# Kernel tuning notes

Measured on AMD Instinct MI355X. Metric: run time of the kernel, lower is better.

## Reference

```python
import math
import jax, jax.numpy as jnp
import numpy as np

HEADS = 16
MODEL = 1024
KEY = 64
VAL = 64
B, S = 4, 2048


def setup_inputs() -> dict:
    key = jax.random.key(0)
    ks = jax.random.split(key, 8)
    queries = jax.random.normal(ks[0], (B, S, MODEL), dtype=jnp.float32)
    keys_ = jax.random.normal(ks[1], (B, S, MODEL), dtype=jnp.float32)
    values = jax.random.normal(ks[2], (B, S, MODEL), dtype=jnp.float32)
    # causal boolean mask, true = attention allowed (every row has >=1 True)
    masks = jnp.broadcast_to(jnp.tril(jnp.ones((S, S), dtype=bool)), (B, S, S))
    lim_in = 1.0 / math.sqrt(MODEL)
    # stacked per-head projection weights, stored as [H, model, head_dim]
    Wq = jax.random.uniform(ks[3], (HEADS, MODEL, KEY), minval=-lim_in, maxval=lim_in, dtype=jnp.float32)
    Wk = jax.random.uniform(ks[4], (HEADS, MODEL, KEY), minval=-lim_in, maxval=lim_in, dtype=jnp.float32)
    Wv = jax.random.uniform(ks[5], (HEADS, MODEL, VAL), minval=-lim_in, maxval=lim_in, dtype=jnp.float32)
    lim_o = 1.0 / math.sqrt(HEADS * VAL)
    Wo = jax.random.uniform(ks[6], (HEADS * VAL, MODEL), minval=-lim_o, maxval=lim_o, dtype=jnp.float32)
    bo = jax.random.uniform(ks[7], (MODEL,), minval=-lim_o, maxval=lim_o, dtype=jnp.float32)
    return {"queries": queries, "keys": keys_, "values": values, "masks": masks,
            "Wq": Wq, "Wk": Wk, "Wv": Wv, "Wo": Wo, "bo": bo}


def reference(queries, keys, values, masks, Wq, Wk, Wv, Wo, bo):
    # per-head projections, batched over heads: [B,S,M] x [H,M,D] -> [B,H,S,D]
    q = jnp.einsum('bsm,hmd->bhsd', queries, Wq)
    k = jnp.einsum('bsm,hmd->bhsd', keys, Wk)
    v = jnp.einsum('bsm,hmd->bhsd', values, Wv)
    scale = 1.0 / math.sqrt(KEY)
    scores = jnp.einsum('bhqd,bhkd->bhqk', q, k) * scale  # [B,H,Q,K]
    scores = jnp.where(masks[:, None, :, :], scores, -jnp.inf)
    weights = jax.nn.softmax(scores, axis=-1)
    out = jnp.einsum('bhqk,bhkv->bhqv', weights, v)  # [B,H,Q,V]
    # concat heads along feature dim (head-major order matches torch concat)
    out = out.transpose(0, 2, 1, 3).reshape(B, S, HEADS * VAL)
    return out @ Wo + bo
```

## Files before the change

### kernel.cpp

```cpp
#include <hip/hip_runtime.h>


typedef __bf16 bf16;
typedef __attribute__((ext_vector_type(8))) __bf16 bf16x8;
typedef __attribute__((ext_vector_type(4))) __bf16 bf16x4;
typedef __attribute__((ext_vector_type(4))) float f32x4;
typedef unsigned int u32;

#define GLB_AS __attribute__((address_space(1)))
#define LDS_AS __attribute__((address_space(3)))

#define L2E 1.44269504088896340736f

static __device__ __forceinline__ void stage_swz(const bf16* __restrict__ g, long ldelem,
                                                 long row0, long col0,
                                                 bf16* lds, int rows, int tid)
{
    const int lane = tid & 63;
    const int wave = tid >> 6;
    const int nch = rows >> 3;
    for (int c = wave; c < nch; c += 4) {
        unsigned o  = ((unsigned)c << 10) + ((unsigned)lane << 4);
        unsigned r  = o >> 7;
        unsigned cb = o & 127u;
        unsigned cs = cb ^ ((r & 7u) << 4);
        const bf16* src = g + (row0 + (long)r) * ldelem + col0 + (long)(cs >> 1);
        char* dst = (char*)lds + ((unsigned)c << 10);
        __builtin_amdgcn_global_load_lds((GLB_AS u32*)src, (LDS_AS u32*)dst, 16, 0, 0);
    }
}

__global__ void cast3(const float4* __restrict__ a, const float4* __restrict__ b,
                      const float4* __restrict__ c,
                      bf16x4* __restrict__ xa, bf16x4* __restrict__ xb,
                      bf16x4* __restrict__ xc)
{
    const int n4 = (8192 * 1024) / 4;
    for (int i = blockIdx.x * blockDim.x + threadIdx.x; i < n4; i += gridDim.x * blockDim.x) {
        float4 v;
        v = a[i]; xa[i] = (bf16x4){(bf16)v.x, (bf16)v.y, (bf16)v.z, (bf16)v.w};
        v = b[i]; xb[i] = (bf16x4){(bf16)v.x, (bf16)v.y, (bf16)v.z, (bf16)v.w};
        v = c[i]; xc[i] = (bf16x4){(bf16)v.x, (bf16)v.y, (bf16)v.z, (bf16)v.w};
    }
}

__global__ void transw(const float* __restrict__ wq, const float* __restrict__ wk,
                       const float* __restrict__ wv, const float* __restrict__ wo,
                       bf16* __restrict__ wqT, bf16* __restrict__ wkT,
                       bf16* __restrict__ wvT, bf16* __restrict__ woT)
{
    __shared__ float t[64][65];
    const int tid = threadIdx.x, bx = blockIdx.x, by = blockIdx.y;
    const float* srcs[3] = {wq, wk, wv};
    bf16* dsts[3] = {wqT, wkT, wvT};
#pragma unroll
    for (int m = 0; m < 3; ++m) {
        const float sc = (m == 0) ? 0.125f : 1.0f;
        for (int i = tid; i < 4096; i += 256) {
            int r = i >> 6, c = i & 63;
            t[c][r] = srcs[m][by * 65536 + (bx * 64 + r) * 64 + c];
        }
        __syncthreads();
        for (int i = tid; i < 4096; i += 256) {
            int r = i >> 6, c = i & 63;
            dsts[m][(long)(by * 64 + r) * 1024 + bx * 64 + c] = (bf16)(t[r][c] * sc);
        }
        __syncthreads();
    }
    for (int i = tid; i < 4096; i += 256) {
        int r = i >> 6, c = i & 63;
        t[c][r] = wo[(long)(bx * 64 + r) * 1024 + by * 64 + c];
    }
    __syncthreads();
    for (int i = tid; i < 4096; i += 256) {
        int r = i >> 6, c = i & 63;
        woT[(long)(by * 64 + r) * 1024 + bx * 64 + c] = (bf16)t[r][c];
    }
}

template<int MODE>
__global__ __launch_bounds__(256, 2) void gemm8k(const bf16* __restrict__ A,
                                                 const bf16* __restrict__ Bt,
                                                 bf16* __restrict__ Cb,
                                                 float* __restrict__ Cf,
                                                 const float* __restrict__ bias)
{
    __shared__ alignas(16) bf16 sA[2][128 * 64];
    __shared__ alignas(16) bf16 sB[2][128 * 64];
    const int tid = threadIdx.x, lane = tid & 63, wave = tid >> 6;
    const int wr = wave >> 1, wc = wave & 1;
    const long row0 = (long)blockIdx.x << 7;
    const long col0 = (long)blockIdx.y << 7;

    f32x4 acc[4][4];
#pragma unroll
    for (int i = 0; i < 4; ++i)
#pragma unroll
        for (int j = 0; j < 4; ++j) acc[i][j] = (f32x4){0.f, 0.f, 0.f, 0.f};

    stage_swz(A,  1024, row0, 0, sA[0], 128, tid);
    stage_swz(Bt, 1024, col0, 0, sB[0], 128, tid);

    for (int kt = 0; kt < 16; ++kt) {
        const int cur = kt & 1;
        __syncthreads();
        if (kt + 1 < 16) {
            stage_swz(A,  1024, row0, (long)(kt + 1) << 6, sA[cur ^ 1], 128, tid);
            stage_swz(Bt, 1024, col0, (long)(kt + 1) << 6, sB[cur ^ 1], 128, tid);
        }
#pragma unroll
        for (int kk = 0; kk < 2; ++kk) {
            bf16x8 af[4], bfr[4];
            const unsigned kb = (unsigned)(kk << 6) + (unsigned)((lane >> 4) << 4);
#pragma unroll
            for (int i = 0; i < 4; ++i) {
                unsigned r = (unsigned)((wr << 6) + (i << 4) + (lane & 15));
                af[i] = *(const bf16x8*)((const char*)sA[cur] + (r << 7) + (kb ^ ((r & 7u) << 4)));
            }
#pragma unroll
            for (int j = 0; j < 4; ++j) {
                unsigned r = (unsigned)((wc << 6) + (j << 4) + (lane & 15));
                bfr[j] = *(const bf16x8*)((const char*)sB[cur] + (r << 7) + (kb ^ ((r & 7u) << 4)));
            }
#pragma unroll
            for (int i = 0; i < 4; ++i)
#pragma unroll
                for (int j = 0; j < 4; ++j)
                    acc[i][j] = __builtin_amdgcn_mfma_f32_16x16x32_bf16(af[i], bfr[j], acc[i][j], 0, 0, 0);
        }
    }

#pragma unroll
    for (int i = 0; i < 4; ++i) {
#pragma unroll
        for (int j = 0; j < 4; ++j) {
#pragma unroll
            for (int rr = 0; rr < 4; ++rr) {
                long row = row0 + (wr << 6) + (i << 4) + ((lane >> 4) << 2) + rr;
                long col = col0 + (wc << 6) + (j << 4) + (lane & 15);
                float v = acc[i][j][rr];
                if constexpr (MODE == 2) {
                    Cf[row * 1024 + col] = v + bias[col];
                } else if constexpr (MODE == 0) {
                    long idx = (((row >> 11) << 4) + (col >> 6)) * 131072 + (row & 2047) * 64 + (col & 63);
                    Cb[idx] = (bf16)v;
                } else {
                    long idx = ((((col >> 11) << 4) + (row >> 6)) * 64 + (row & 63)) * 2048 + (col & 2047);
                    Cb[idx] = (bf16)v;
                }
            }
        }
    }
}

__global__ __launch_bounds__(256, 2) void attn(const bf16* __restrict__ q,
                                               const bf16* __restrict__ k,
                                               const bf16* __restrict__ vT,
                                               bf16* __restrict__ o)
{
    __shared__ alignas(16) bf16 sK[2][64 * 64];
    __shared__ alignas(16) bf16 sV[2][64 * 64];
    __shared__ alignas(16) bf16 sP[4][32 * 72];
    const int tid = threadIdx.x, lane = tid & 63, wave = tid >> 6;
    const int bid = blockIdx.x;
    const int hb = ((bid & 7) << 3) + ((bid >> 3) & 7);
    const int pair = bid >> 6;
    const int h = hb & 15, b = hb >> 4;
    const bf16* qh = q  + (long)hb * 131072;
    const bf16* kh = k  + (long)hb * 131072;
    const bf16* vh = vT + (long)hb * 131072;

    bf16x8 vone;
#pragma unroll
    for (int i = 0; i < 8; ++i) vone[i] = (bf16)1.0f;

    for (int half = 0; half < 2; ++half) {
        const int qt = half ? (15 - pair) : pair;
        const int qw = (qt << 7) + (wave << 5);

        bf16x8 aq[2][2];
#pragma unroll
        for (int mf = 0; mf < 2; ++mf)
#pragma unroll
            for (int kk = 0; kk < 2; ++kk)
                aq[mf][kk] = *(const bf16x8*)(qh + (long)(qw + (mf << 4) + (lane & 15)) * 64
                                                 + (kk << 5) + ((lane >> 4) << 3));

        f32x4 accO[2][4], accOl[2];
        float mrow[2][4];
#pragma unroll
        for (int mf = 0; mf < 2; ++mf) {
#pragma unroll
            for (int nf = 0; nf < 4; ++nf) accO[mf][nf] = (f32x4){0.f, 0.f, 0.f, 0.f};
            accOl[mf] = (f32x4){0.f, 0.f, 0.f, 0.f};
#pragma unroll
            for (int rr = 0; rr < 4; ++rr) mrow[mf][rr] = -1e30f;
        }

        const int nkv = (qt << 1) + 2;
        __syncthreads();
        stage_swz(kh, 64,   0, 0, sK[0], 64, tid);
        stage_swz(vh, 2048, 0, 0, sV[0], 64, tid);

        for (int kvt = 0; kvt < nkv; ++kvt) {
            const int cur = kvt & 1;
            const int kv0 = kvt << 6;
            __syncthreads();
            if (kvt + 1 < nkv) {
                stage_swz(kh, 64,   (long)(kv0 + 64), 0, sK[cur ^ 1], 64, tid);
                stage_swz(vh, 2048, 0, (long)(kv0 + 64), sV[cur ^ 1], 64, tid);
            }
            if (kv0 > qw + 31) continue;

            f32x4 s[2][4];
#pragma unroll
            for (int mf = 0; mf < 2; ++mf)
#pragma unroll
                for (int nf = 0; nf < 4; ++nf) s[mf][nf] = (f32x4){0.f, 0.f, 0.f, 0.f};
#pragma unroll
            for (int kk = 0; kk < 2; ++kk) {
                bf16x8 bk[4];
                const unsigned kb = (unsigned)(kk << 6) + (unsigned)((lane >> 4) << 4);
#pragma unroll
                for (int nf = 0; nf < 4; ++nf) {
                    unsigned r = (unsigned)((nf << 4) + (lane & 15));
                    bk[nf] = *(const bf16x8*)((const char*)sK[cur] + (r << 7) + (kb ^ ((r & 7u) << 4)));
                }
#pragma unroll
                for (int mf = 0; mf < 2; ++mf)
#pragma unroll
                    for (int nf = 0; nf < 4; ++nf)
                        s[mf][nf] = __builtin_amdgcn_mfma_f32_16x16x32_bf16(aq[mf][kk], bk[nf], s[mf][nf], 0, 0, 0);
            }

            if (kv0 + 63 > qw) {
#pragma unroll
                for (int mf = 0; mf < 2; ++mf)
#pragma unroll
                    for (int rr = 0; rr < 4; ++rr) {
                        const int ra = qw + (mf << 4) + ((lane >> 4) << 2) + rr;
#pragma unroll
                        for (int nf = 0; nf < 4; ++nf)
                            if ((kv0 + (nf << 4) + (lane & 15)) > ra) s[mf][nf][rr] = -1e30f;
                    }
            }

#pragma unroll
            for (int mf = 0; mf < 2; ++mf) {
#pragma unroll
                for (int rr = 0; rr < 4; ++rr) {
                    float mt = fmaxf(fmaxf(s[mf][0][rr], s[mf][1][rr]), fmaxf(s[mf][2][rr], s[mf][3][rr]));
                    mt = fmaxf(mt, __shfl_xor(mt, 1));
                    mt = fmaxf(mt, __shfl_xor(mt, 2));
                    mt = fmaxf(mt, __shfl_xor(mt, 4));
                    mt = fmaxf(mt, __shfl_xor(mt, 8));
                    if (mt > mrow[mf][rr]) {
                        const float cf = __builtin_exp2f((mrow[mf][rr] - mt) * L2E);
                        mrow[mf][rr] = mt;
                        accOl[mf][rr] *= cf;
#pragma unroll
                        for (int nf = 0; nf < 4; ++nf) accO[mf][nf][rr] *= cf;
                    }
                    const float m2 = mrow[mf][rr] * L2E;
#pragma unroll
                    for (int nf = 0; nf < 4; ++nf)
                        s[mf][nf][rr] = __builtin_exp2f(__builtin_fmaf(s[mf][nf][rr], L2E, -m2));
                }
            }

            bf16* pw = &sP[wave][0];
#pragma unroll
            for (int mf = 0; mf < 2; ++mf)
#pragma unroll
                for (int nf = 0; nf < 4; ++nf)
#pragma unroll
                    for (int rr = 0; rr < 4; ++rr)
                        pw[((mf << 4) + ((lane >> 4) << 2) + rr) * 72 + (nf << 4) + (lane & 15)] =
                            (bf16)s[mf][nf][rr];

#pragma unroll
            for (int kk = 0; kk < 2; ++kk) {
                bf16x8 pa[2], bv[4];
#pragma unroll
                for (int mf = 0; mf < 2; ++mf)
                    pa[mf] = *(const bf16x8*)(pw + ((mf << 4) + (lane & 15)) * 72
                                                 + (kk << 5) + ((lane >> 4) << 3));
                const unsigned kb = (unsigned)(kk << 6) + (unsigned)((lane >> 4) << 4);
#pragma unroll
                for (int nf = 0; nf < 4; ++nf) {
                    unsigned r = (unsigned)((nf << 4) + (lane & 15));
                    bv[nf] = *(const bf16x8*)((const char*)sV[cur] + (r << 7) + (kb ^ ((r & 7u) << 4)));
                }
#pragma unroll
                for (int mf = 0; mf < 2; ++mf) {
#pragma unroll
                    for (int nf = 0; nf < 4; ++nf)
                        accO[mf][nf] = __builtin_amdgcn_mfma_f32_16x16x32_bf16(pa[mf], bv[nf], accO[mf][nf], 0, 0, 0);
                    accOl[mf] = __builtin_amdgcn_mfma_f32_16x16x32_bf16(pa[mf], vone, accOl[mf], 0, 0, 0);
                }
            }
        }

#pragma unroll
        for (int mf = 0; mf < 2; ++mf)
#pragma unroll
            for (int rr = 0; rr < 4; ++rr) {
                const float inv = 1.f / accOl[mf][rr];
                const long ra = qw + (mf << 4) + ((lane >> 4) << 2) + rr;
#pragma unroll
                for (int nf = 0; nf < 4; ++nf)
                    o[((long)b * 2048 + ra) * 1024 + (h << 6) + (nf << 4) + (lane & 15)] =
                        (bf16)(accO[mf][nf][rr] * inv);
            }
    }
}

extern "C" void kernel_launch(void* const* d_in, const int* in_sizes, int n_in,
                              void* d_out, int out_size, void* d_ws, size_t ws_size,
                              hipStream_t stream)
{
    const float* queries = (const float*)d_in[0];
    const float* keys    = (const float*)d_in[1];
    const float* values  = (const float*)d_in[2];
    const float* Wq = (const float*)d_in[4];
    const float* Wk = (const float*)d_in[5];
    const float* Wv = (const float*)d_in[6];
    const float* Wo = (const float*)d_in[7];
    const float* bo = (const float*)d_in[8];
    float* out = (float*)d_out;

    bf16* Xq  = (bf16*)d_ws;
    bf16* Xk  = Xq  + 8388608;
    bf16* Xv  = Xk  + 8388608;
    bf16* WqT = Xv  + 8388608;
    bf16* WkT = WqT + 1048576;
    bf16* WvT = WkT + 1048576;
    bf16* WoT = WvT + 1048576;
    bf16* qp  = WoT + 1048576;
    bf16* kp  = qp  + 8388608;
    bf16* vTp = Xq;
    bf16* ao  = Xk;
    if (ws_size < (size_t)92274688) return;

    cast3<<<dim3(2048), dim3(256), 0, stream>>>((const float4*)queries, (const float4*)keys,
                                                (const float4*)values,
                                                (bf16x4*)Xq, (bf16x4*)Xk, (bf16x4*)Xv);
    transw<<<dim3(16, 16), dim3(256), 0, stream>>>(Wq, Wk, Wv, Wo, WqT, WkT, WvT, WoT);
    gemm8k<0><<<dim3(64, 8), dim3(256), 0, stream>>>(Xq, WqT, qp,  nullptr, nullptr);
    gemm8k<0><<<dim3(64, 8), dim3(256), 0, stream>>>(Xk, WkT, kp,  nullptr, nullptr);
    gemm8k<3><<<dim3(8, 64), dim3(256), 0, stream>>>(WvT, Xv, vTp, nullptr, nullptr);
    attn<<<dim3(512), dim3(256), 0, stream>>>(qp, kp, vTp, ao);
    gemm8k<2><<<dim3(64, 8), dim3(256), 0, stream>>>(ao, WoT, nullptr, out, bo);
}
```

Measured before the change: 441.0 us.

## Merge Q/K/V projection GEMMs into one launch, single-buffer LDS for higher occupancy

Fuses the three separate projection GEMM launches into a single 1536-block kernel that dispatches by blockIdx.y, so all three projections share one wave of blocks instead of three launches with tails. The LDS double buffer is dropped in favour of a single buffer with two barriers per k-step, halving shared memory per block and raising launch bounds to three blocks per CU. The output GEMM gets the same single-buffer treatment. The exchange is that global-to-LDS loads no longer overlap with MFMA work within a block, and the code relies on the extra resident blocks to hide that latency.

Measured after the change: 440.3 us. About the same (-0.2%).

```diff
diff --git a/kernel.cpp b/kernel.cpp
--- a/kernel.cpp
+++ b/kernel.cpp
@@ -79,18 +79,16 @@
 }
 
 template<int MODE>
-__global__ __launch_bounds__(256, 2) void gemm8k(const bf16* __restrict__ A,
+static __device__ __forceinline__ void gemm_body(const bf16* __restrict__ A,
                                                  const bf16* __restrict__ Bt,
                                                  bf16* __restrict__ Cb,
                                                  float* __restrict__ Cf,
-                                                 const float* __restrict__ bias)
-{
-    __shared__ alignas(16) bf16 sA[2][128 * 64];
-    __shared__ alignas(16) bf16 sB[2][128 * 64];
+                                                 const float* __restrict__ bias,
+                                                 long row0, long col0,
+                                                 bf16* sA, bf16* sB)
+{
     const int tid = threadIdx.x, lane = tid & 63, wave = tid >> 6;
     const int wr = wave >> 1, wc = wave & 1;
-    const long row0 = (long)blockIdx.x << 7;
-    const long col0 = (long)blockIdx.y << 7;
 
     f32x4 acc[4][4];
 #pragma unroll
@@ -98,16 +96,11 @@
 #pragma unroll
         for (int j = 0; j < 4; ++j) acc[i][j] = (f32x4){0.f, 0.f, 0.f, 0.f};
 
-    stage_swz(A,  1024, row0, 0, sA[0], 128, tid);
-    stage_swz(Bt, 1024, col0, 0, sB[0], 128, tid);
-
     for (int kt = 0; kt < 16; ++kt) {
-        const int cur = kt & 1;
-        __syncthreads();
-        if (kt + 1 < 16) {
-            stage_swz(A,  1024, row0, (long)(kt + 1) << 6, sA[cur ^ 1], 128, tid);
-            stage_swz(Bt, 1024, col0, (long)(kt + 1) << 6, sB[cur ^ 1], 128, tid);
-        }
+        __syncthreads();
+        stage_swz(A,  1024, row0, (long)kt << 6, sA, 128, tid);
+        stage_swz(Bt, 1024, col0, (long)kt << 6, sB, 128, tid);
+        __syncthreads();
 #pragma unroll
         for (int kk = 0; kk < 2; ++kk) {
             bf16x8 af[4], bfr[4];
@@ -115,12 +108,12 @@
 #pragma unroll
             for (int i = 0; i < 4; ++i) {
                 unsigned r = (unsigned)((wr << 6) + (i << 4) + (lane & 15));
-                af[i] = *(const bf16x8*)((const char*)sA[cur] + (r << 7) + (kb ^ ((r & 7u) << 4)));
+                af[i] = *(const bf16x8*)((const char*)sA + (r << 7) + (kb ^ ((r & 7u) << 4)));
             }
 #pragma unroll
             for (int j = 0; j < 4; ++j) {
                 unsigned r = (unsigned)((wc << 6) + (j << 4) + (lane & 15));
-                bfr[j] = *(const bf16x8*)((const char*)sB[cur] + (r << 7) + (kb ^ ((r & 7u) << 4)));
+                bfr[j] = *(const bf16x8*)((const char*)sB + (r << 7) + (kb ^ ((r & 7u) << 4)));
             }
 #pragma unroll
             for (int i = 0; i < 4; ++i)
@@ -153,6 +146,29 @@
     }
 }
 
+__global__ __launch_bounds__(256, 3) void gemm_qkv(const bf16* __restrict__ Xq, const bf16* __restrict__ WqT, bf16* __restrict__ qp,
+                                                   const bf16* __restrict__ Xk, const bf16* __restrict__ WkT, bf16* __restrict__ kp,
+                                                   const bf16* __restrict__ WvT, const bf16* __restrict__ Xv, bf16* __restrict__ vTp)
+{
+    __shared__ alignas(16) bf16 sA[128 * 64];
+    __shared__ alignas(16) bf16 sB[128 * 64];
+    const int bx = blockIdx.x;
+    if (blockIdx.y == 0)
+        gemm_body<0>(Xq, WqT, qp, nullptr, nullptr, (long)(bx >> 3) << 7, (long)(bx & 7) << 7, sA, sB);
+    else if (blockIdx.y == 1)
+        gemm_body<0>(Xk, WkT, kp, nullptr, nullptr, (long)(bx >> 3) << 7, (long)(bx & 7) << 7, sA, sB);
+    else
+        gemm_body<3>(WvT, Xv, vTp, nullptr, nullptr, (long)(bx & 7) << 7, (long)(bx >> 3) << 7, sA, sB);
+}
+
+__global__ __launch_bounds__(256, 3) void gemm_out(const bf16* __restrict__ A, const bf16* __restrict__ Bt,
+                                                   float* __restrict__ Cf, const float* __restrict__ bias)
+{
+    __shared__ alignas(16) bf16 sA[128 * 64];
+    __shared__ alignas(16) bf16 sB[128 * 64];
+    gemm_body<2>(A, Bt, nullptr, Cf, bias, (long)blockIdx.x << 7, (long)blockIdx.y << 7, sA, sB);
+}
+
 __global__ __launch_bounds__(256, 2) void attn(const bf16* __restrict__ q,
                                                const bf16* __restrict__ k,
                                                const bf16* __restrict__ vT,
@@ -346,9 +362,7 @@
                                                 (const float4*)values,
                                                 (bf16x4*)Xq, (bf16x4*)Xk, (bf16x4*)Xv);
     transw<<<dim3(16, 16), dim3(256), 0, stream>>>(Wq, Wk, Wv, Wo, WqT, WkT, WvT, WoT);
-    gemm8k<0><<<dim3(64, 8), dim3(256), 0, stream>>>(Xq, WqT, qp,  nullptr, nullptr);
-    gemm8k<0><<<dim3(64, 8), dim3(256), 0, stream>>>(Xk, WkT, kp,  nullptr, nullptr);
-    gemm8k<3><<<dim3(8, 64), dim3(256), 0, stream>>>(WvT, Xv, vTp, nullptr, nullptr);
+    gemm_qkv<<<dim3(512, 3), dim3(256), 0, stream>>>(Xq, WqT, qp, Xk, WkT, kp, WvT, Xv, vTp);
     attn<<<dim3(512), dim3(256), 0, stream>>>(qp, kp, vTp, ao);
-    gemm8k<2><<<dim3(64, 8), dim3(256), 0, stream>>>(ao, WoT, nullptr, out, bo);
-}
+    gemm_out<<<dim3(64, 8), dim3(256), 0, stream>>>(ao, WoT, out, bo);
+}
```
